# Performance work log

Hardware: AMD Instinct MI355X
Metric: run time of the kernel (lower is better)

The kernel has to match this reference:

```python
import jax, jax.numpy as jnp
import numpy as np

N_SRC, N_DST, E = 100000, 50000, 1000000
IN_F, H, D = 256, 4, 32
NEG_SLOPE = 0.2


def setup_inputs() -> dict:
    key = jax.random.key(0)
    k = jax.random.split(key, 7)
    x = jax.random.normal(k[0], (N_SRC, IN_F), dtype=jnp.float32)
    # scale weights so exp() of attention logits stays well-conditioned
    fc_w = jax.random.normal(k[1], (H * D, IN_F), dtype=jnp.float32) * (1.0 / np.sqrt(IN_F))
    attn_l = jax.random.normal(k[2], (1, H, D), dtype=jnp.float32) * 0.1
    attn_r = jax.random.normal(k[3], (1, H, D), dtype=jnp.float32) * 0.1
    src_idx = jax.random.randint(k[4], (E,), 0, N_SRC, dtype=jnp.int32)
    dst_idx = jax.random.randint(k[5], (E,), 0, N_DST, dtype=jnp.int32)
    dst_node_ids = jax.random.randint(k[6], (N_DST,), 0, N_SRC, dtype=jnp.int32)
    return {"x": x, "fc_w": fc_w, "attn_l": attn_l, "attn_r": attn_r,
            "src_idx": src_idx, "dst_idx": dst_idx, "dst_node_ids": dst_node_ids}


def reference(x, fc_w, attn_l, attn_r, src_idx, dst_idx, dst_node_ids):
    # fc: [N_src, in] @ [in, H*D] -> [N_src, H, D]
    h = (x @ fc_w.T).reshape(-1, H, D)
    # per-node, per-head attention scalars
    el = jnp.einsum('nhd,ohd->nh', h, attn_l)            # [N_src, H]
    h_dst = h[dst_node_ids]                               # self_gather -> [N_dst, H, D]
    er = jnp.einsum('nhd,ohd->nh', h_dst, attn_r)        # [N_dst, H]
    # apply_edge: e = el[src] + er[dst], then leaky_relu + exp (edge softmax numerator)
    e = el[src_idx] + er[dst_idx]                         # [E, H]
    e = jnp.where(e >= 0, e, NEG_SLOPE * e)
    exp_e = jnp.exp(e)
    # apply_node: segment-sum denominators over destination nodes
    sum_exp = jax.ops.segment_sum(exp_e, dst_idx, num_segments=N_DST)  # [N_dst, H]
    att = exp_e / sum_exp[dst_idx]                        # [E, H]
    # attention_gather: weighted scatter-add of source features to dst nodes
    msg = att[:, :, None] * h[src_idx]                    # [E, H, D]
    out = jax.ops.segment_sum(msg, dst_idx, num_segments=N_DST)        # [N_dst, H, D]
    return out.reshape(N_DST, H * D)
```

## Files before the change

### kernel.cpp

```cpp
#include <hip/hip_runtime.h>
#include <hip/hip_bf16.h>

#define N_SRC_N  100000
#define N_DST_N  50000
#define NE       1000000
#define IN_F     256
#define NH       4
#define ND       32
#define HD       128
#define NEG_SLOPE 0.2f

#define DPB      32
#define NB       1563
#define CAP      1024

typedef __attribute__((ext_vector_type(8))) short short8v;
typedef __attribute__((ext_vector_type(4))) short short4v;
typedef __attribute__((ext_vector_type(4))) float f32x4;

__device__ __forceinline__ short f2bf(float f) {
    __hip_bfloat16 h = __float2bfloat16(f);
    return *reinterpret_cast<short*>(&h);
}
__device__ __forceinline__ float bflo(unsigned u) { return __uint_as_float(u << 16); }
__device__ __forceinline__ float bfhi(unsigned u) { return __uint_as_float(u & 0xffff0000u); }

__global__ __launch_bounds__(256) void cvt_w(const float* __restrict__ w,
                                             short* __restrict__ wb)
{
    int i4 = blockIdx.x * 256 + threadIdx.x;
    if (i4 < (HD * IN_F) / 4) {
        f32x4 v = ((const f32x4*)w)[i4];
        short4v s;
        s[0] = f2bf(v[0]); s[1] = f2bf(v[1]); s[2] = f2bf(v[2]); s[3] = f2bf(v[3]);
        ((short4v*)wb)[i4] = s;
    }
}

__global__ __launch_bounds__(512, 4) void gemm_fc_mfma(
    const float* __restrict__ x, const short* __restrict__ wb,
    const float* __restrict__ al, short* __restrict__ hb,
    float* __restrict__ el)
{
    __shared__ short wlds[HD * IN_F];

    const int tid = threadIdx.x;
    {
        int row = tid >> 2, qt = tid & 3;
#pragma unroll
        for (int c = 0; c < 8; ++c) {
            int chunk = qt * 8 + c;
            short8v v = *(const short8v*)(wb + row * IN_F + chunk * 8);
            int boff = (chunk * 16) ^ ((row & 7) << 4);
            *(short8v*)((char*)wlds + row * 512 + boff) = v;
        }
    }
    __syncthreads();

    const int w  = tid >> 6;
    const int l  = tid & 63;
    const int lr = l & 15;
    const int lk = l >> 4;

    float alv[8];
#pragma unroll
    for (int ct = 0; ct < 8; ++ct) alv[ct] = al[ct * 16 + lr];

    const int wave_id = blockIdx.x * 8 + w;
    for (int tile = wave_id; tile < N_SRC_N / 16; tile += 4096) {
        const int row0 = tile * 16;
        const float* xp = x + (size_t)(row0 + lr) * IN_F + lk * 8;

        f32x4 a[16];
#pragma unroll
        for (int kk = 0; kk < 8; ++kk) {
            a[2 * kk]     = *(const f32x4*)(xp + kk * 32);
            a[2 * kk + 1] = *(const f32x4*)(xp + kk * 32 + 4);
        }
        __builtin_amdgcn_sched_barrier(0);

        f32x4 acc[8];
#pragma unroll
        for (int ct = 0; ct < 8; ++ct) acc[ct] = (f32x4){0.f, 0.f, 0.f, 0.f};

#pragma unroll
        for (int kk = 0; kk < 8; ++kk) {
            f32x4 u0 = a[2 * kk], u1 = a[2 * kk + 1];
            short8v af;
            af[0] = f2bf(u0[0]); af[1] = f2bf(u0[1]);
            af[2] = f2bf(u0[2]); af[3] = f2bf(u0[3]);
            af[4] = f2bf(u1[0]); af[5] = f2bf(u1[1]);
            af[6] = f2bf(u1[2]); af[7] = f2bf(u1[3]);
            const int boff = (kk * 64 + lk * 16) ^ ((lr & 7) << 4);
#pragma unroll
            for (int ct = 0; ct < 8; ++ct) {
                short8v bf = *(const short8v*)((const char*)wlds
                                               + (ct * 16 + lr) * 512 + boff);
                acc[ct] = __builtin_amdgcn_mfma_f32_16x16x32_bf16(af, bf, acc[ct], 0, 0, 0);
            }
        }

#pragma unroll
        for (int r = 0; r < 4; ++r) {
            short* hp = hb + (size_t)(row0 + lk * 4 + r) * HD + lr;
#pragma unroll
            for (int ct = 0; ct < 8; ++ct) hp[ct * 16] = f2bf(acc[ct][r]);
        }

#pragma unroll
        for (int h = 0; h < 4; ++h) {
            float p[4];
#pragma unroll
            for (int r = 0; r < 4; ++r)
                p[r] = acc[2 * h][r] * alv[2 * h] + acc[2 * h + 1][r] * alv[2 * h + 1];
#pragma unroll
            for (int o = 1; o < 16; o <<= 1) {
#pragma unroll
                for (int r = 0; r < 4; ++r) p[r] += __shfl_xor(p[r], o, 64);
            }
            if (lr == 0) {
#pragma unroll
                for (int r = 0; r < 4; ++r)
                    el[(row0 + lk * 4 + r) * NH + h] = p[r];
            }
        }
    }
}

__global__ __launch_bounds__(256) void bucket_hist(
    const int4* __restrict__ dst4, int* __restrict__ bcnt, int n4)
{
    __shared__ int lh[NB];
    for (int i = threadIdx.x; i < NB; i += 256) lh[i] = 0;
    __syncthreads();
#pragma unroll
    for (int q = 0; q < 4; ++q) {
        int e4 = blockIdx.x * 1024 + q * 256 + threadIdx.x;
        if (e4 < n4) {
            int4 v = dst4[e4];
            atomicAdd(&lh[v.x >> 5], 1); atomicAdd(&lh[v.y >> 5], 1);
            atomicAdd(&lh[v.z >> 5], 1); atomicAdd(&lh[v.w >> 5], 1);
        }
    }
    __syncthreads();
    for (int i = threadIdx.x; i < NB; i += 256) {
        int c = lh[i];
        if (c > 0) atomicAdd(&bcnt[i], c);
    }
}

__global__ __launch_bounds__(1024) void bucket_scan(
    const int* __restrict__ bcnt, int* __restrict__ boff, int* __restrict__ bcur, int n)
{
    int tid = threadIdx.x;
    int i0 = 2 * tid, i1 = 2 * tid + 1;
    int a = (i0 < n) ? bcnt[i0] : 0;
    int c = (i1 < n) ? bcnt[i1] : 0;
    int s = a + c, v = s;
#pragma unroll
    for (int o = 1; o < 64; o <<= 1) {
        int t = __shfl_up(v, o, 64);
        if ((tid & 63) >= o) v += t;
    }
    __shared__ int ws[16];
    if ((tid & 63) == 63) ws[tid >> 6] = v;
    __syncthreads();
    int add = 0;
    for (int q = 0; q < (tid >> 6); ++q) add += ws[q];
    int excl = v - s + add;
    if (i0 < n) { boff[i0] = excl;     bcur[i0] = excl; }
    if (i1 < n) { boff[i1] = excl + a; bcur[i1] = excl + a; }
}

__global__ __launch_bounds__(256) void partition(
    const int4* __restrict__ src4, const int4* __restrict__ dst4,
    int* __restrict__ bcur, int* __restrict__ ebuf, int n4)
{
    __shared__ int lh[NB];
    __shared__ int base[NB];
    for (int i = threadIdx.x; i < NB; i += 256) lh[i] = 0;
    __syncthreads();
    int4 sv[8], dv[8];
#pragma unroll
    for (int q = 0; q < 8; ++q) {
        int e4 = blockIdx.x * 2048 + q * 256 + threadIdx.x;
        if (e4 < n4) {
            sv[q] = src4[e4]; dv[q] = dst4[e4];
            atomicAdd(&lh[dv[q].x >> 5], 1); atomicAdd(&lh[dv[q].y >> 5], 1);
            atomicAdd(&lh[dv[q].z >> 5], 1); atomicAdd(&lh[dv[q].w >> 5], 1);
        } else {
            dv[q].x = -1;
        }
    }
    __syncthreads();
    for (int i = threadIdx.x; i < NB; i += 256) {
        int cnt = lh[i];
        base[i] = (cnt > 0) ? atomicAdd(&bcur[i], cnt) : 0;
        lh[i] = 0;
    }
    __syncthreads();
#pragma unroll
    for (int q = 0; q < 8; ++q) {
        if (dv[q].x < 0) continue;
        int ss[4] = {sv[q].x, sv[q].y, sv[q].z, sv[q].w};
        int dd[4] = {dv[q].x, dv[q].y, dv[q].z, dv[q].w};
#pragma unroll
        for (int j = 0; j < 4; ++j) {
            int b = dd[j] >> 5;
            int off = atomicAdd(&lh[b], 1);
            ebuf[base[b] + off] = ss[j] | ((dd[j] & 31) << 17);
        }
    }
}

__global__ __launch_bounds__(256) void gat_gather(
    const short* __restrict__ hb, const float* __restrict__ el,
    const float* __restrict__ ar, const int* __restrict__ dnid,
    const int* __restrict__ ebuf, const int* __restrict__ bcnt,
    const int* __restrict__ boff, float* __restrict__ out, int ndst)
{
    __shared__ int stage_[CAP];
    __shared__ int ssrc[CAP];
    __shared__ int lh[DPB];
    __shared__ int loff[DPB + 1];
    __shared__ int curs[DPB];

    const int b = blockIdx.x;
    const int tid = threadIdx.x;
    const int cnt = bcnt[b];
    const int gbase = boff[b];
    const int lcnt = (cnt < CAP) ? cnt : CAP;

    if (tid < DPB) lh[tid] = 0;
    __syncthreads();
    for (int i = tid; i < lcnt; i += 256) {
        int p = ebuf[gbase + i];
        stage_[i] = p;
        atomicAdd(&lh[(p >> 17) & 31], 1);
    }
    __syncthreads();
    if (tid < DPB) {
        int v = lh[tid];
#pragma unroll
        for (int o = 1; o < 32; o <<= 1) {
            int t = __shfl_up(v, o, 64);
            if (tid >= o) v += t;
        }
        loff[tid + 1] = v;
        if (tid == 0) loff[0] = 0;
    }
    __syncthreads();
    if (tid < DPB) curs[tid] = loff[tid];
    __syncthreads();
    for (int i = tid; i < lcnt; i += 256) {
        int p = stage_[i];
        int dl = (p >> 17) & 31;
        int pos = atomicAdd(&curs[dl], 1);
        ssrc[pos] = (p & 0x1FFFF) << 8;
    }
    __syncthreads();

    const int wv = tid >> 6;
    const int l  = tid & 63;
    const int head = l >> 4;
    const char* hbase = (const char*)hb + 4 * l;
    const char* ebase = (const char*)el + head * 4;
    const float ar0 = ar[2 * l], ar1 = ar[2 * l + 1];

    for (int dl = wv; dl < DPB; dl += 4) {
        int d = b * DPB + dl;
        if (d >= ndst) continue;
        int j0 = loff[dl], j1 = loff[dl + 1];

        int nid = dnid[d];
        unsigned ue = *(const unsigned*)(hbase + (size_t)nid * 256);
        float erv = bflo(ue) * ar0 + bfhi(ue) * ar1;
#pragma unroll
        for (int o = 1; o < 16; o <<= 1) erv += __shfl_xor(erv, o, 64);

        float sumA = 0.f, sumB = 0.f;
        float acc0A = 0.f, acc1A = 0.f, acc0B = 0.f, acc1B = 0.f;
        int j = j0;
        for (; j + 8 <= j1; j += 8) {
            int off[8]; unsigned u[8]; float ev[8];
#pragma unroll
            for (int q = 0; q < 8; ++q) off[q] = ssrc[j + q];
#pragma unroll
            for (int q = 0; q < 8; ++q)
                u[q] = *(const unsigned*)(hbase + off[q]);
#pragma unroll
            for (int q = 0; q < 8; ++q)
                ev[q] = *(const float*)(ebase + (off[q] >> 4));
#pragma unroll
            for (int q = 0; q < 8; ++q) {
                float e = ev[q] + erv;
                e = fmaxf(e, NEG_SLOPE * e);
                float wq = __expf(e);
                if (q & 1) {
                    sumB += wq;
                    acc0B = fmaf(wq, bflo(u[q]), acc0B);
                    acc1B = fmaf(wq, bfhi(u[q]), acc1B);
                } else {
                    sumA += wq;
                    acc0A = fmaf(wq, bflo(u[q]), acc0A);
                    acc1A = fmaf(wq, bfhi(u[q]), acc1A);
                }
            }
        }
        for (; j < j1; ++j) {
            int off0 = ssrc[j];
            unsigned u0 = *(const unsigned*)(hbase + off0);
            float e0 = *(const float*)(ebase + (off0 >> 4)) + erv;
            e0 = fmaxf(e0, NEG_SLOPE * e0);
            float w0 = __expf(e0);
            sumA += w0;
            acc0A = fmaf(w0, bflo(u0), acc0A); acc1A = fmaf(w0, bfhi(u0), acc1A);
        }
        if (cnt > CAP) {
            for (int t = CAP; t < cnt; ++t) {
                int p = ebuf[gbase + t];
                if (((p >> 17) & 31) == dl) {
                    int off0 = (p & 0x1FFFF) << 8;
                    unsigned u0 = *(const unsigned*)(hbase + off0);
                    float e0 = *(const float*)(ebase + (off0 >> 4)) + erv;
                    e0 = fmaxf(e0, NEG_SLOPE * e0);
                    float w0 = __expf(e0);
                    sumA += w0;
                    acc0A = fmaf(w0, bflo(u0), acc0A); acc1A = fmaf(w0, bfhi(u0), acc1A);
                }
            }
        }
        float sum = sumA + sumB;
        bool any = (j1 > j0) || (cnt > CAP);
        float inv = any ? 1.f / sum : 0.f;
        float2 o2 = make_float2((acc0A + acc0B) * inv, (acc1A + acc1B) * inv);
        *(float2*)(out + (size_t)d * HD + 2 * l) = o2;
    }
}

extern "C" void kernel_launch(void* const* d_in, const int* in_sizes, int n_in,
                              void* d_out, int out_size, void* d_ws, size_t ws_size,
                              hipStream_t stream)
{
    const float* x   = (const float*)d_in[0];
    const float* fw  = (const float*)d_in[1];
    const float* al  = (const float*)d_in[2];
    const float* ar  = (const float*)d_in[3];
    const int*   src = (const int*)d_in[4];
    const int*   dst = (const int*)d_in[5];
    const int*   dnid= (const int*)d_in[6];
    float* out = (float*)d_out;

    char* ws = (char*)d_ws;
    size_t off = 0;
    auto alloc = [&](size_t bytes) -> void* {
        void* p = ws + off;
        off = (off + bytes + 255) & ~(size_t)255;
        return p;
    };
    short* hb   = (short*)alloc((size_t)N_SRC_N * HD * sizeof(short));
    short* wb   = (short*)alloc((size_t)HD * IN_F * sizeof(short));
    float* el   = (float*)alloc((size_t)N_SRC_N * NH * sizeof(float));
    int*   ebuf = (int*)alloc((size_t)NE * sizeof(int));
    int*   bcnt = (int*)alloc((size_t)NB * sizeof(int));
    int*   boff = (int*)alloc((size_t)NB * sizeof(int));
    int*   bcur = (int*)alloc((size_t)NB * sizeof(int));

    hipMemsetAsync(bcnt, 0, (size_t)NB * sizeof(int), stream);

    cvt_w<<<(HD * IN_F / 4 + 255) / 256, 256, 0, stream>>>(fw, wb);
    gemm_fc_mfma<<<512, 512, 0, stream>>>(x, wb, al, hb, el);
    bucket_hist<<<(NE / 4 + 1023) / 1024, 256, 0, stream>>>((const int4*)dst, bcnt, NE / 4);
    bucket_scan<<<1, 1024, 0, stream>>>(bcnt, boff, bcur, NB);
    partition<<<(NE / 4 + 2047) / 2048, 256, 0, stream>>>((const int4*)src, (const int4*)dst,
                                                          bcur, ebuf, NE / 4);
    gat_gather<<<NB, 256, 0, stream>>>(hb, el, ar, dnid, ebuf, bcnt, boff, out, N_DST_N);
}
```

Before: 125.9 us.

## Precompute per-edge attention weights in shared memory during the bucket scatter

The er dot products for all 32 destinations in a block are now computed up front and stored in shared memory. The per-edge exp weights for all four heads are computed once per edge during the local counting-sort scatter and written to a shared weights array. Before, each of the 64 lanes in a wave recomputed leaky_relu and exp for its head and loaded el per edge. The gather loop now only reads the weights from LDS. The cost is about 16KB more shared memory per block, which may lower occupancy, plus an extra el vector load in the scatter phase.

Result: slower. 140.8 us (+11.8%).

```diff
diff --git a/kernel.cpp b/kernel.cpp
--- a/kernel.cpp
+++ b/kernel.cpp
@@ -219,11 +219,13 @@
     const int* __restrict__ ebuf, const int* __restrict__ bcnt,
     const int* __restrict__ boff, float* __restrict__ out, int ndst)
 {
-    __shared__ int stage_[CAP];
-    __shared__ int ssrc[CAP];
-    __shared__ int lh[DPB];
-    __shared__ int loff[DPB + 1];
-    __shared__ int curs[DPB];
+    __shared__ int   stage_[CAP];
+    __shared__ int   ssrc[CAP];
+    __shared__ float wts[CAP][4];
+    __shared__ float erl[DPB][4];
+    __shared__ int   lh[DPB];
+    __shared__ int   loff[DPB + 1];
+    __shared__ int   curs[DPB];
 
     const int b = blockIdx.x;
     const int tid = threadIdx.x;
@@ -231,6 +233,12 @@
     const int gbase = boff[b];
     const int lcnt = (cnt < CAP) ? cnt : CAP;
 
+    const int wv = tid >> 6;
+    const int l  = tid & 63;
+    const int head = l >> 4;
+    const float ar0 = ar[2 * l], ar1 = ar[2 * l + 1];
+    const char* hbase = (const char*)hb + 4 * l;
+
     if (tid < DPB) lh[tid] = 0;
     __syncthreads();
     for (int i = tid; i < lcnt; i += 256) {
@@ -238,7 +246,20 @@
         stage_[i] = p;
         atomicAdd(&lh[(p >> 17) & 31], 1);
     }
-    __syncthreads();
+
+#pragma unroll
+    for (int q = 0; q < 8; ++q) {
+        int dl = wv * 8 + q;
+        int d = b * DPB + dl;
+        int nid = (d < ndst) ? dnid[d] : 0;
+        unsigned ue = *(const unsigned*)(hbase + (size_t)nid * 256);
+        float erv = bflo(ue) * ar0 + bfhi(ue) * ar1;
+#pragma unroll
+        for (int o = 1; o < 16; o <<= 1) erv += __shfl_xor(erv, o, 64);
+        if ((l & 15) == 0) erl[dl][head] = erv;
+    }
+    __syncthreads();
+
     if (tid < DPB) {
         int v = lh[tid];
 #pragma unroll
@@ -252,67 +273,59 @@
     __syncthreads();
     if (tid < DPB) curs[tid] = loff[tid];
     __syncthreads();
+
     for (int i = tid; i < lcnt; i += 256) {
         int p = stage_[i];
+        int src = p & 0x1FFFF;
         int dl = (p >> 17) & 31;
         int pos = atomicAdd(&curs[dl], 1);
-        ssrc[pos] = (p & 0x1FFFF) << 8;
-    }
-    __syncthreads();
-
-    const int wv = tid >> 6;
-    const int l  = tid & 63;
-    const int head = l >> 4;
-    const char* hbase = (const char*)hb + 4 * l;
-    const char* ebase = (const char*)el + head * 4;
-    const float ar0 = ar[2 * l], ar1 = ar[2 * l + 1];
+        ssrc[pos] = src << 8;
+        f32x4 elv = *(const f32x4*)(el + src * NH);
+        f32x4 w4;
+#pragma unroll
+        for (int h = 0; h < 4; ++h) {
+            float e = elv[h] + erl[dl][h];
+            e = fmaxf(e, NEG_SLOPE * e);
+            w4[h] = __expf(e);
+        }
+        *(f32x4*)&wts[pos][0] = w4;
+    }
+    __syncthreads();
 
     for (int dl = wv; dl < DPB; dl += 4) {
         int d = b * DPB + dl;
         if (d >= ndst) continue;
         int j0 = loff[dl], j1 = loff[dl + 1];
 
-        int nid = dnid[d];
-        unsigned ue = *(const unsigned*)(hbase + (size_t)nid * 256);
-        float erv = bflo(ue) * ar0 + bfhi(ue) * ar1;
-#pragma unroll
-        for (int o = 1; o < 16; o <<= 1) erv += __shfl_xor(erv, o, 64);
-
         float sumA = 0.f, sumB = 0.f;
         float acc0A = 0.f, acc1A = 0.f, acc0B = 0.f, acc1B = 0.f;
         int j = j0;
         for (; j + 8 <= j1; j += 8) {
-            int off[8]; unsigned u[8]; float ev[8];
+            int off[8]; unsigned u[8]; float wq[8];
 #pragma unroll
             for (int q = 0; q < 8; ++q) off[q] = ssrc[j + q];
 #pragma unroll
             for (int q = 0; q < 8; ++q)
                 u[q] = *(const unsigned*)(hbase + off[q]);
 #pragma unroll
-            for (int q = 0; q < 8; ++q)
-                ev[q] = *(const float*)(ebase + (off[q] >> 4));
+            for (int q = 0; q < 8; ++q) wq[q] = wts[j + q][head];
 #pragma unroll
             for (int q = 0; q < 8; ++q) {
-                float e = ev[q] + erv;
-                e = fmaxf(e, NEG_SLOPE * e);
-                float wq = __expf(e);
                 if (q & 1) {
-                    sumB += wq;
-                    acc0B = fmaf(wq, bflo(u[q]), acc0B);
-                    acc1B = fmaf(wq, bfhi(u[q]), acc1B);
+                    sumB += wq[q];
+                    acc0B = fmaf(wq[q], bflo(u[q]), acc0B);
+                    acc1B = fmaf(wq[q], bfhi(u[q]), acc1B);
                 } else {
-                    sumA += wq;
-                    acc0A = fmaf(wq, bflo(u[q]), acc0A);
-                    acc1A = fmaf(wq, bfhi(u[q]), acc1A);
+                    sumA += wq[q];
+                    acc0A = fmaf(wq[q], bflo(u[q]), acc0A);
+                    acc1A = fmaf(wq[q], bfhi(u[q]), acc1A);
                 }
             }
         }
         for (; j < j1; ++j) {
             int off0 = ssrc[j];
             unsigned u0 = *(const unsigned*)(hbase + off0);
-            float e0 = *(const float*)(ebase + (off0 >> 4)) + erv;
-            e0 = fmaxf(e0, NEG_SLOPE * e0);
-            float w0 = __expf(e0);
+            float w0 = wts[j][head];
             sumA += w0;
             acc0A = fmaf(w0, bflo(u0), acc0A); acc1A = fmaf(w0, bfhi(u0), acc1A);
         }
@@ -320,9 +333,9 @@
             for (int t = CAP; t < cnt; ++t) {
                 int p = ebuf[gbase + t];
                 if (((p >> 17) & 31) == dl) {
-                    int off0 = (p & 0x1FFFF) << 8;
-                    unsigned u0 = *(const unsigned*)(hbase + off0);
-                    float e0 = *(const float*)(ebase + (off0 >> 4)) + erv;
+                    int src = p & 0x1FFFF;
+                    unsigned u0 = *(const unsigned*)(hbase + (size_t)src * 256);
+                    float e0 = el[src * NH + head] + erl[dl][head];
                     e0 = fmaxf(e0, NEG_SLOPE * e0);
                     float w0 = __expf(e0);
                     sumA += w0;
```
